# Kernel optimization log

Measured on AMD Instinct MI355X. Metric: run time of the kernel, lower is better.

## Reference

```python
import jax, jax.numpy as jnp
import numpy as np

CANVAS_W = 1024.0
CANVAS_H = 1024.0
EPS = 1e-8
GOLDEN = 1.618
ALIGN_THRESH = 5.0


def _mse(p, t):
    return jnp.mean((p - t) ** 2)


def _smooth_l1(p, t):
    d = jnp.abs(p - t)
    return jnp.mean(jnp.where(d < 1.0, 0.5 * d * d, d - 0.5))


def setup_inputs() -> dict:
    key = jax.random.key(0)
    k1, k2, k3, k4 = jax.random.split(key, 4)
    B, N, D = 64, 256, 6
    return {
        "predicted_noise": jax.random.normal(k1, (B, N, D), dtype=jnp.float32),
        "target_noise": jax.random.normal(k2, (B, N, D), dtype=jnp.float32),
        "predicted_layout": jax.random.normal(k3, (B, N, D), dtype=jnp.float32),
        "target_layout": jax.random.normal(k4, (B, N, D), dtype=jnp.float32),
        "element_mask": jnp.ones((B, N), dtype=jnp.float32),
    }


def _iou_loss(pred, target):
    # boxes are (x, y, w, h)
    px1, py1 = pred[..., 0], pred[..., 1]
    px2, py2 = px1 + pred[..., 2], py1 + pred[..., 3]
    tx1, ty1 = target[..., 0], target[..., 1]
    tx2, ty2 = tx1 + target[..., 2], ty1 + target[..., 3]
    inter = jnp.maximum(jnp.minimum(px2, tx2) - jnp.maximum(px1, tx1), 0.0) * \
            jnp.maximum(jnp.minimum(py2, ty2) - jnp.maximum(py1, ty1), 0.0)
    pa = pred[..., 2] * pred[..., 3]
    ta = target[..., 2] * target[..., 3]
    iou = inter / (pa + ta - inter + EPS)
    return jnp.mean(1.0 - iou)


def _loss(predicted_noise, target_noise, predicted_layout, target_layout, element_mask):
    B, N, _ = predicted_noise.shape
    mask3 = element_mask[..., None]  # [B,N,1]
    pn = predicted_noise * mask3
    tn = target_noise * mask3
    pl = predicted_layout * mask3
    tl = target_layout * mask3

    npairs = N * (N - 1) / 2.0
    tri = jnp.triu(jnp.ones((N, N), dtype=pl.dtype), k=1)  # i<j pair mask
    pair_valid = element_mask[:, :, None] * element_mask[:, None, :]  # [B,N,N]

    # ---- noise loss (SmoothL1) ----
    noise_loss = _smooth_l1(pn, tn)

    # ---- position loss: MSE + 0.5*IoU ----
    position_loss = _mse(pl[..., :4], tl[..., :4]) + 0.5 * _iou_loss(pl[..., :4], tl[..., :4])

    # ---- layer loss: MSE + 0.3*pairwise ranking BCE ----
    p_layer, t_layer = pl[..., 4], tl[..., 4]
    diff = p_layer[:, None, :] - p_layer[:, :, None]          # [b,i,j] = p_j - p_i
    y = (t_layer[:, :, None] < t_layer[:, None, :]).astype(pl.dtype)
    # BCE(sigmoid(diff), y): -log sigmoid(d)=softplus(-d); torch clamps log terms at 100
    bce = y * jnp.minimum(jax.nn.softplus(-diff), 100.0) + \
          (1.0 - y) * jnp.minimum(jax.nn.softplus(diff), 100.0)
    ranking = jnp.sum(bce * tri) / (B * npairs)
    layer_loss = _mse(p_layer, t_layer) + 0.3 * ranking

    # ---- confidence loss ----
    confidence_loss = _mse(pl[..., 5], tl[..., 5])

    # ---- aesthetic loss ----
    aspect = pl[..., 2] / (pl[..., 3] + EPS)
    golden = jnp.mean(jnp.abs(aspect - GOLDEN))
    areas = pl[..., 2] * pl[..., 3] * element_mask
    size_harm = jnp.mean(jnp.std(areas, axis=1, ddof=1)) / (jnp.mean(areas) + EPS)
    cx = (pl[..., 0] + pl[..., 2] / 2) * element_mask
    cy = (pl[..., 1] + pl[..., 3] / 2) * element_mask
    valid_count = jnp.sum(element_mask, axis=1, keepdims=True)  # [B,1]
    # NOTE: faithful to original broadcasting ([B] / [B,1] -> [B,B])
    ocx = jnp.sum(cx, axis=1) / (valid_count + EPS)
    ocy = jnp.sum(cy, axis=1) / (valid_count + EPS)
    balance = jnp.mean(jnp.abs(ocx - CANVAS_W / 2) / (CANVAS_W / 2) +
                       jnp.abs(ocy - CANVAS_H / 2) / (CANVAS_H / 2))
    aesthetic_loss = 0.1 * golden + 0.2 * size_harm + 0.15 * balance

    # ---- overlap loss (pairwise) ----
    x1, y1, w, h = pl[..., 0], pl[..., 1], pl[..., 2], pl[..., 3]
    x2, y2 = x1 + w, y1 + h
    iw = jnp.maximum(jnp.minimum(x2[:, :, None], x2[:, None, :]) -
                     jnp.maximum(x1[:, :, None], x1[:, None, :]), 0.0)
    ih = jnp.maximum(jnp.minimum(y2[:, :, None], y2[:, None, :]) -
                     jnp.maximum(y1[:, :, None], y1[:, None, :]), 0.0)
    area = w * h
    min_area = jnp.minimum(area[:, :, None], area[:, None, :])
    overlap_ratio = (iw * ih) / (min_area + EPS) * pair_valid
    overlap_loss = jnp.sum(overlap_ratio * tri) / (B * npairs)

    # ---- alignment loss (6 edge types, pairwise) ----
    edges = jnp.stack([x1, x2, y1, y2, x1 + w / 2, y1 + h / 2], axis=0)  # [6,B,N]
    dist = jnp.abs(edges[:, :, :, None] - edges[:, :, None, :])          # [6,B,N,N]
    pen = jnp.where(dist < ALIGN_THRESH, dist / ALIGN_THRESH, 0.0) * pair_valid[None]
    alignment_loss = jnp.sum(pen * tri) / (B * 6.0 * npairs)

    total = (noise_loss + 1.0 * position_loss + 0.5 * layer_loss +
             0.3 * confidence_loss + 0.2 * aesthetic_loss +
             0.8 * overlap_loss + 0.4 * alignment_loss)
    return total


def reference(predicted_noise, target_noise, predicted_layout, target_layout, element_mask):
    return _loss(predicted_noise, target_noise, predicted_layout, target_layout, element_mask)
```

## Files before the change

kernel.cpp:

```cpp
#include <hip/hip_runtime.h>
#include <math.h>

#define NB 64
#define NN 256
#define NPAIRS 32640.0f
#define EPSF 1e-8f

#define PB(q) ((q) * 64)
#define PWBASE 704

__device__ __forceinline__ float block_sum(float v, float* sred) {
    const int tid = threadIdx.x;
    #pragma unroll
    for (int off = 32; off > 0; off >>= 1) v += __shfl_down(v, off, 64);
    __syncthreads();
    if ((tid & 63) == 0) sred[tid >> 6] = v;
    __syncthreads();
    return sred[0] + sred[1] + sred[2] + sred[3];
}

__device__ __forceinline__ void block_sum3(float a, float b, float c, float* sred,
                                           float& ra, float& rb, float& rc) {
    const int tid = threadIdx.x;
    #pragma unroll
    for (int off = 32; off > 0; off >>= 1) {
        a += __shfl_down(a, off, 64);
        b += __shfl_down(b, off, 64);
        c += __shfl_down(c, off, 64);
    }
    __syncthreads();
    if ((tid & 63) == 0) {
        const int w = tid >> 6;
        sred[w] = a; sred[4 + w] = b; sred[8 + w] = c;
    }
    __syncthreads();
    ra = sred[0] + sred[1] + sred[2]  + sred[3];
    rb = sred[4] + sred[5] + sred[6]  + sred[7];
    rc = sred[8] + sred[9] + sred[10] + sred[11];
}

__device__ __forceinline__ float wave_sum(float v) {
    #pragma unroll
    for (int off = 32; off > 0; off >>= 1) v += __shfl_down(v, off, 64);
    return v;
}

__global__ __launch_bounds__(256, 8) void loss_main(
    const float* __restrict__ pn, const float* __restrict__ tn,
    const float* __restrict__ pl, const float* __restrict__ tl,
    const float* __restrict__ mask, float* __restrict__ ws)
{
    __shared__ float4 sA[NN], sB[NN];
    __shared__ float2 sC[NN];
    __shared__ float sred[12];

    const int b     = blockIdx.x >> 5;
    const int chunk = blockIdx.x & 31;
    const int i     = threadIdx.x;
    const int e     = b * NN + i;
    const float m   = mask[e];

    const float2* pl2 = (const float2*)pl;
    const float2* tl2 = (const float2*)tl;
    const int r2 = e * 3;
    const float2 pla = pl2[r2 + 0], plb = pl2[r2 + 1], plc = pl2[r2 + 2];
    const float2 tlc = tl2[r2 + 2];

    const float p0 = pla.x * m, p1 = pla.y * m,
                p2 = plb.x * m, p3 = plb.y * m,
                p4 = plc.x * m, p5 = plc.y * m;
    const float t4 = tlc.x * m, t5 = tlc.y * m;

    const float x2v = p0 + p2, y2v = p1 + p3;
    const float areav = p2 * p3;
    const float cxe = p0 + 0.5f * p2, cye = p1 + 0.5f * p3;

    sA[i] = make_float4(p0, p1, x2v, y2v);
    sB[i] = make_float4(cxe, cye, areav, p4);
    sC[i] = make_float2(t4, m);
    __syncthreads();

    float rank = 0.f, ovl = 0.f, aln = 0.f;
    const int dd0 = chunk * 4 + 1;
    #pragma unroll
    for (int k = 0; k < 4; ++k) {
        const int dd = dd0 + k;
        int j = (i + dd) & 255;
        if (dd == 128 && i >= 128) continue;
        float4 aj = sA[j];
        float4 bj = sB[j];
        float2 cj = sC[j];
        float pv = m * cj.y;
        float ow = fmaxf(fminf(x2v, aj.z) - fmaxf(p0, aj.x), 0.f);
        float oh = fmaxf(fminf(y2v, aj.w) - fmaxf(p1, aj.y), 0.f);
        ovl += ow * oh * pv * __builtin_amdgcn_rcpf(fminf(areav, bj.z) + EPSF);
        float pen = 0.f, d;
        d = fabsf(p0  - aj.x); pen += (d < 5.f) ? d : 0.f;
        d = fabsf(x2v - aj.z); pen += (d < 5.f) ? d : 0.f;
        d = fabsf(p1  - aj.y); pen += (d < 5.f) ? d : 0.f;
        d = fabsf(y2v - aj.w); pen += (d < 5.f) ? d : 0.f;
        d = fabsf(cxe - bj.x); pen += (d < 5.f) ? d : 0.f;
        d = fabsf(cye - bj.y); pen += (d < 5.f) ? d : 0.f;
        aln += pen * (0.2f * pv);
        bool ilt = (i < j);
        float dlo = ilt ? (bj.w - p4) : (p4 - bj.w);
        bool ylt  = ilt ? (t4 < cj.x) : (cj.x < t4);
        float z   = ylt ? -dlo : dlo;
        float sp  = __logf(1.f + __expf(-fabsf(z))) + fmaxf(z, 0.f);
        rank += fminf(sp, 100.f);
    }

    {
        float sr, so, sa;
        block_sum3(rank, ovl, aln, sred, sr, so, sa);
        if (i == 0) {
            *(float4*)(ws + PWBASE + blockIdx.x * 4) = make_float4(sr, so, sa, 0.f);
        }
    }

    float v = 0.f;
    bool have = true;
    switch (chunk) {
    case 0: {
        const float2* pn2 = (const float2*)pn;
        const float2* tn2 = (const float2*)tn;
        float noise = 0.f;
        #pragma unroll
        for (int k = 0; k < 3; ++k) {
            float2 a = pn2[r2 + k], bb = tn2[r2 + k];
            float d0 = fabsf(a.x * m - bb.x * m);
            float d1 = fabsf(a.y * m - bb.y * m);
            noise += (d0 < 1.f) ? 0.5f * d0 * d0 : d0 - 0.5f;
            noise += (d1 < 1.f) ? 0.5f * d1 * d1 : d1 - 0.5f;
        }
        v = noise;
        break; }
    case 1: {
        const float2 tla = tl2[r2 + 0], tlb = tl2[r2 + 1];
        const float t0 = tla.x * m, t1 = tla.y * m,
                    t2 = tlb.x * m, t3 = tlb.y * m;
        v = (p0 - t0) * (p0 - t0) + (p1 - t1) * (p1 - t1)
          + (p2 - t2) * (p2 - t2) + (p3 - t3) * (p3 - t3);
        break; }
    case 2: {
        const float2 tla = tl2[r2 + 0], tlb = tl2[r2 + 1];
        const float t0 = tla.x * m, t1 = tla.y * m,
                    t2 = tlb.x * m, t3 = tlb.y * m;
        const float tx2 = t0 + t2, ty2 = t1 + t3;
        float iw = fmaxf(fminf(x2v, tx2) - fmaxf(p0, t0), 0.f);
        float ih = fmaxf(fminf(y2v, ty2) - fmaxf(p1, t1), 0.f);
        float inter = iw * ih;
        v = 1.f - inter / (areav + t2 * t3 - inter + EPSF);
        break; }
    case 3: v = (p4 - t4) * (p4 - t4); break;
    case 4: v = (p5 - t5) * (p5 - t5); break;
    case 5: v = fabsf(p2 / (p3 + EPSF) - 1.618f); break;
    case 6: v = areav * m; break;
    case 7: { float a = areav * m; v = a * a; break; }
    case 8: v = cxe * m; break;
    case 9: v = cye * m; break;
    case 10: v = m; break;
    default: have = false; break;
    }
    if (have) {
        float s = block_sum(v, sred);
        if (i == 0) ws[PB(chunk) + b] = s;
    }
}

__global__ __launch_bounds__(256) void loss_final(
    const float* __restrict__ ws, float* __restrict__ out)
{
    __shared__ float sred[12];
    const int t = threadIdx.x;

    float v_rank = 0.f, v_ovl = 0.f, v_aln = 0.f;
    #pragma unroll
    for (int k = 0; k < 8; ++k) {
        float4 p = *(const float4*)(ws + PWBASE + (k * 256 + t) * 4);
        v_rank += p.x; v_ovl += p.y; v_aln += p.z;
    }
    float S_rank, S_ovl, S_aln;
    block_sum3(v_rank, v_ovl, v_aln, sred, S_rank, S_ovl, S_aln);

    if (t < 64) {
        float v_noise = ws[PB(0) + t];
        float v_pos   = ws[PB(1) + t];
        float v_iou   = ws[PB(2) + t];
        float v_lm    = ws[PB(3) + t];
        float v_cf    = ws[PB(4) + t];
        float v_go    = ws[PB(5) + t];
        float v_ar    = ws[PB(6) + t];
        float a2      = ws[PB(7) + t];
        float v_cx    = ws[PB(8) + t];
        float v_cy    = ws[PB(9) + t];
        float v_vc    = ws[PB(10) + t];
        float var   = (a2 - v_ar * v_ar * (1.f / 256.f)) * (1.f / 255.f);
        float v_std = sqrtf(fmaxf(var, 0.f));

        float inv = 1.f / (v_vc + EPSF);
        float v_bal = 0.f;
        for (int j = 0; j < NB; ++j) {
            float cxj = __shfl(v_cx, j, 64);
            float cyj = __shfl(v_cy, j, 64);
            v_bal += fabsf(cxj * inv - 512.f) * (1.f / 512.f)
                   + fabsf(cyj * inv - 512.f) * (1.f / 512.f);
        }

        float S_noise = wave_sum(v_noise);
        float S_pos   = wave_sum(v_pos);
        float S_iou   = wave_sum(v_iou);
        float S_lm    = wave_sum(v_lm);
        float S_cf    = wave_sum(v_cf);
        float S_go    = wave_sum(v_go);
        float S_ar    = wave_sum(v_ar);
        float S_std   = wave_sum(v_std);
        float S_bal   = wave_sum(v_bal);

        if (t == 0) {
            const float BN = 64.f * 256.f;
            float noise_loss = S_noise / (BN * 6.f);
            float position   = S_pos / (BN * 4.f) + 0.5f * (S_iou / BN);
            float layer      = S_lm / BN + 0.3f * (S_rank / (64.f * NPAIRS));
            float conf       = S_cf / BN;
            float golden     = S_go / BN;
            float size_harm  = (S_std / 64.f) / (S_ar / BN + EPSF);
            float balance    = S_bal / 4096.f;
            float aes        = 0.1f * golden + 0.2f * size_harm + 0.15f * balance;
            float ovl        = S_ovl / (64.f * NPAIRS);
            float aln        = S_aln / (64.f * 6.f * NPAIRS);
            out[0] = noise_loss + position + 0.5f * layer + 0.3f * conf
                   + 0.2f * aes + 0.8f * ovl + 0.4f * aln;
        }
    }
}

extern "C" void kernel_launch(void* const* d_in, const int* in_sizes, int n_in,
                              void* d_out, int out_size, void* d_ws, size_t ws_size,
                              hipStream_t stream) {
    const float* pn   = (const float*)d_in[0];
    const float* tn   = (const float*)d_in[1];
    const float* pl   = (const float*)d_in[2];
    const float* tl   = (const float*)d_in[3];
    const float* mask = (const float*)d_in[4];
    float* ws  = (float*)d_ws;
    float* out = (float*)d_out;
    hipLaunchKernelGGL(loss_main, dim3(2048), dim3(256), 0, stream,
                       pn, tn, pl, tl, mask, ws);
    hipLaunchKernelGGL(loss_final, dim3(1), dim3(256), 0, stream, ws, out);
}
```

Measured before the change: 72.69 us.

## Fuse final reduction into main kernel via last-block atomic ticket

Merges the two-kernel pipeline into one kernel: each block writes its partials, bumps an atomic ticket, and the last block to arrive performs the final cross-block reduction. The per-chunk scalar sum is also folded into a single four-way block reduction instead of a separate one. This removes the second kernel launch and one block-level reduction, but adds a memset launch to reset the ticket, an atomic plus fence per block, and coherent loads in the tail block. Launch bounds lose the occupancy hint of 8.

```diff
diff --git a/kernel.cpp b/kernel.cpp
--- a/kernel.cpp
+++ b/kernel.cpp
@@ -8,25 +8,45 @@
 
 #define PB(q) ((q) * 64)
 #define PWBASE 704
-
-__device__ __forceinline__ float block_sum(float v, float* sred) {
-    const int tid = threadIdx.x;
+#define TICKET_OFF 16384
+
+__device__ __forceinline__ float wave_sum(float v) {
     #pragma unroll
     for (int off = 32; off > 0; off >>= 1) v += __shfl_down(v, off, 64);
-    __syncthreads();
-    if ((tid & 63) == 0) sred[tid >> 6] = v;
-    __syncthreads();
-    return sred[0] + sred[1] + sred[2] + sred[3];
-}
-
-__device__ __forceinline__ void block_sum3(float a, float b, float c, float* sred,
-                                           float& ra, float& rb, float& rc) {
+    return v;
+}
+
+__device__ __forceinline__ void block_sum4(float a, float b, float c, float d,
+                                           float* sred,
+                                           float& ra, float& rb, float& rc, float& rd) {
     const int tid = threadIdx.x;
     #pragma unroll
     for (int off = 32; off > 0; off >>= 1) {
         a += __shfl_down(a, off, 64);
         b += __shfl_down(b, off, 64);
         c += __shfl_down(c, off, 64);
+        d += __shfl_down(d, off, 64);
+    }
+    __syncthreads();
+    if ((tid & 63) == 0) {
+        const int w = tid >> 6;
+        sred[w] = a; sred[4 + w] = b; sred[8 + w] = c; sred[12 + w] = d;
+    }
+    __syncthreads();
+    ra = sred[0]  + sred[1]  + sred[2]  + sred[3];
+    rb = sred[4]  + sred[5]  + sred[6]  + sred[7];
+    rc = sred[8]  + sred[9]  + sred[10] + sred[11];
+    rd = sred[12] + sred[13] + sred[14] + sred[15];
+}
+
+__device__ __forceinline__ void block_sum3(float a, float b, float c, float* sred,
+                                           float& ra, float& rb, float& rc) {
+    const int tid = threadIdx.x;
+    #pragma unroll
+    for (int off = 32; off > 0; off >>= 1) {
+        a += __shfl_down(a, off, 64);
+        b += __shfl_down(b, off, 64);
+        c += __shfl_down(c, off, 64);
     }
     __syncthreads();
     if ((tid & 63) == 0) {
@@ -39,20 +59,20 @@
     rc = sred[8] + sred[9] + sred[10] + sred[11];
 }
 
-__device__ __forceinline__ float wave_sum(float v) {
-    #pragma unroll
-    for (int off = 32; off > 0; off >>= 1) v += __shfl_down(v, off, 64);
-    return v;
-}
-
-__global__ __launch_bounds__(256, 8) void loss_main(
+__device__ __forceinline__ float ws_cload(const float* p) {
+    return __hip_atomic_load(p, __ATOMIC_RELAXED, __HIP_MEMORY_SCOPE_AGENT);
+}
+
+__global__ __launch_bounds__(256) void loss_fused(
     const float* __restrict__ pn, const float* __restrict__ tn,
     const float* __restrict__ pl, const float* __restrict__ tl,
-    const float* __restrict__ mask, float* __restrict__ ws)
+    const float* __restrict__ mask, float* __restrict__ ws,
+    float* __restrict__ out)
 {
     __shared__ float4 sA[NN], sB[NN];
     __shared__ float2 sC[NN];
-    __shared__ float sred[12];
+    __shared__ float sred[16];
+    __shared__ int winflag;
 
     const int b     = blockIdx.x >> 5;
     const int chunk = blockIdx.x & 31;
@@ -80,46 +100,8 @@
     sC[i] = make_float2(t4, m);
     __syncthreads();
 
-    float rank = 0.f, ovl = 0.f, aln = 0.f;
-    const int dd0 = chunk * 4 + 1;
-    #pragma unroll
-    for (int k = 0; k < 4; ++k) {
-        const int dd = dd0 + k;
-        int j = (i + dd) & 255;
-        if (dd == 128 && i >= 128) continue;
-        float4 aj = sA[j];
-        float4 bj = sB[j];
-        float2 cj = sC[j];
-        float pv = m * cj.y;
-        float ow = fmaxf(fminf(x2v, aj.z) - fmaxf(p0, aj.x), 0.f);
-        float oh = fmaxf(fminf(y2v, aj.w) - fmaxf(p1, aj.y), 0.f);
-        ovl += ow * oh * pv * __builtin_amdgcn_rcpf(fminf(areav, bj.z) + EPSF);
-        float pen = 0.f, d;
-        d = fabsf(p0  - aj.x); pen += (d < 5.f) ? d : 0.f;
-        d = fabsf(x2v - aj.z); pen += (d < 5.f) ? d : 0.f;
-        d = fabsf(p1  - aj.y); pen += (d < 5.f) ? d : 0.f;
-        d = fabsf(y2v - aj.w); pen += (d < 5.f) ? d : 0.f;
-        d = fabsf(cxe - bj.x); pen += (d < 5.f) ? d : 0.f;
-        d = fabsf(cye - bj.y); pen += (d < 5.f) ? d : 0.f;
-        aln += pen * (0.2f * pv);
-        bool ilt = (i < j);
-        float dlo = ilt ? (bj.w - p4) : (p4 - bj.w);
-        bool ylt  = ilt ? (t4 < cj.x) : (cj.x < t4);
-        float z   = ylt ? -dlo : dlo;
-        float sp  = __logf(1.f + __expf(-fabsf(z))) + fmaxf(z, 0.f);
-        rank += fminf(sp, 100.f);
-    }
-
-    {
-        float sr, so, sa;
-        block_sum3(rank, ovl, aln, sred, sr, so, sa);
-        if (i == 0) {
-            *(float4*)(ws + PWBASE + blockIdx.x * 4) = make_float4(sr, so, sa, 0.f);
-        }
-    }
-
     float v = 0.f;
-    bool have = true;
+    const bool have = (chunk < 11);
     switch (chunk) {
     case 0: {
         const float2* pn2 = (const float2*)pn;
@@ -160,41 +142,77 @@
     case 8: v = cxe * m; break;
     case 9: v = cye * m; break;
     case 10: v = m; break;
-    default: have = false; break;
-    }
-    if (have) {
-        float s = block_sum(v, sred);
-        if (i == 0) ws[PB(chunk) + b] = s;
-    }
-}
-
-__global__ __launch_bounds__(256) void loss_final(
-    const float* __restrict__ ws, float* __restrict__ out)
-{
-    __shared__ float sred[12];
-    const int t = threadIdx.x;
+    default: break;
+    }
+
+    float rank = 0.f, ovl = 0.f, aln = 0.f;
+    const int dd0 = chunk * 4 + 1;
+    #pragma unroll
+    for (int k = 0; k < 4; ++k) {
+        const int dd = dd0 + k;
+        int j = (i + dd) & 255;
+        if (dd == 128 && i >= 128) continue;
+        float4 aj = sA[j];
+        float4 bj = sB[j];
+        float2 cj = sC[j];
+        float pv = m * cj.y;
+        float ow = fmaxf(fminf(x2v, aj.z) - fmaxf(p0, aj.x), 0.f);
+        float oh = fmaxf(fminf(y2v, aj.w) - fmaxf(p1, aj.y), 0.f);
+        ovl += ow * oh * pv * __builtin_amdgcn_rcpf(fminf(areav, bj.z) + EPSF);
+        float pen = 0.f, d;
+        d = fabsf(p0  - aj.x); pen += (d < 5.f) ? d : 0.f;
+        d = fabsf(x2v - aj.z); pen += (d < 5.f) ? d : 0.f;
+        d = fabsf(p1  - aj.y); pen += (d < 5.f) ? d : 0.f;
+        d = fabsf(y2v - aj.w); pen += (d < 5.f) ? d : 0.f;
+        d = fabsf(cxe - bj.x); pen += (d < 5.f) ? d : 0.f;
+        d = fabsf(cye - bj.y); pen += (d < 5.f) ? d : 0.f;
+        aln += pen * (0.2f * pv);
+        bool ilt = (i < j);
+        float dlo = ilt ? (bj.w - p4) : (p4 - bj.w);
+        bool ylt  = ilt ? (t4 < cj.x) : (cj.x < t4);
+        float z   = ylt ? -dlo : dlo;
+        float sp  = __logf(1.f + __expf(-fabsf(z))) + fmaxf(z, 0.f);
+        rank += fminf(sp, 100.f);
+    }
+
+    float sr, so, sa, sv;
+    block_sum4(rank, ovl, aln, v, sred, sr, so, sa, sv);
+
+    if (i == 0) {
+        *(float4*)(ws + PWBASE + blockIdx.x * 4) = make_float4(sr, so, sa, 0.f);
+        if (have) ws[PB(chunk) + b] = sv;
+        __threadfence();
+        unsigned old = atomicAdd((unsigned*)(ws + TICKET_OFF), 1u);
+        winflag = (old == 2047u) ? 1 : 0;
+    }
+    __syncthreads();
+    if (!winflag) return;
+
+    const int t = i;
 
     float v_rank = 0.f, v_ovl = 0.f, v_aln = 0.f;
     #pragma unroll
     for (int k = 0; k < 8; ++k) {
-        float4 p = *(const float4*)(ws + PWBASE + (k * 256 + t) * 4);
-        v_rank += p.x; v_ovl += p.y; v_aln += p.z;
+        const float* p = ws + PWBASE + (k * 256 + t) * 4;
+        v_rank += ws_cload(p + 0);
+        v_ovl  += ws_cload(p + 1);
+        v_aln  += ws_cload(p + 2);
     }
     float S_rank, S_ovl, S_aln;
     block_sum3(v_rank, v_ovl, v_aln, sred, S_rank, S_ovl, S_aln);
 
     if (t < 64) {
-        float v_noise = ws[PB(0) + t];
-        float v_pos   = ws[PB(1) + t];
-        float v_iou   = ws[PB(2) + t];
-        float v_lm    = ws[PB(3) + t];
-        float v_cf    = ws[PB(4) + t];
-        float v_go    = ws[PB(5) + t];
-        float v_ar    = ws[PB(6) + t];
-        float a2      = ws[PB(7) + t];
-        float v_cx    = ws[PB(8) + t];
-        float v_cy    = ws[PB(9) + t];
-        float v_vc    = ws[PB(10) + t];
+        float v_noise = ws_cload(ws + PB(0) + t);
+        float v_pos   = ws_cload(ws + PB(1) + t);
+        float v_iou   = ws_cload(ws + PB(2) + t);
+        float v_lm    = ws_cload(ws + PB(3) + t);
+        float v_cf    = ws_cload(ws + PB(4) + t);
+        float v_go    = ws_cload(ws + PB(5) + t);
+        float v_ar    = ws_cload(ws + PB(6) + t);
+        float a2      = ws_cload(ws + PB(7) + t);
+        float v_cx    = ws_cload(ws + PB(8) + t);
+        float v_cy    = ws_cload(ws + PB(9) + t);
+        float v_vc    = ws_cload(ws + PB(10) + t);
         float var   = (a2 - v_ar * v_ar * (1.f / 256.f)) * (1.f / 255.f);
         float v_std = sqrtf(fmaxf(var, 0.f));
 
@@ -245,7 +263,7 @@
     const float* mask = (const float*)d_in[4];
     float* ws  = (float*)d_ws;
     float* out = (float*)d_out;
-    hipLaunchKernelGGL(loss_main, dim3(2048), dim3(256), 0, stream,
-                       pn, tn, pl, tl, mask, ws);
-    hipLaunchKernelGGL(loss_final, dim3(1), dim3(256), 0, stream, ws, out);
-}
+    hipMemsetAsync((char*)d_ws + TICKET_OFF * sizeof(float), 0, 4, stream);
+    hipLaunchKernelGGL(loss_fused, dim3(2048), dim3(256), 0, stream,
+                       pn, tn, pl, tl, mask, ws, out);
+}
```

Measured after the change: 112.2 us. +54.4%, slower.
